# Kernel optimization log

Hardware: AMD Instinct MI355X
Metric: run time of the kernel (lower is better)

## Reference

```python
import jax, jax.numpy as jnp
import numpy as np

EPS = 1e-5
NEG_SLOPE = 0.2

def _bn(x, g, be, m, v):
    # inference-mode BatchNorm1d over the channel (last) dim
    return (x - m) * jax.lax.rsqrt(v + EPS) * g + be

def _lrelu(x):
    return jnp.where(x >= 0, x, NEG_SLOPE * x)

def setup_inputs() -> dict:
    key = jax.random.key(0)
    ks = jax.random.split(key, 32)
    B, N, M = 2, 65536, 16
    C_RAW, C_IN, C_RO, C_NB, C_OUT = 10, 32, 32, 64, 64
    i = iter(range(32))
    def nrm(shape, s=1.0):
        return jax.random.normal(ks[next(i)], shape, dtype=jnp.float32) * s
    def pos(shape):
        return jax.random.uniform(ks[next(i)], shape, dtype=jnp.float32)
    inp = {}
    inp['feature'] = nrm((B, N, C_IN))
    inp['raw_nb_fea'] = nrm((B, N, M, C_RAW))
    inp['neighbors_idx'] = jax.random.randint(ks[next(i)], (B, N, M), 0, N, dtype=jnp.int32)
    inp['w_raw'] = nrm((C_RAW, C_RO), 0.3); inp['b_raw'] = nrm((C_RO,), 0.1)
    inp['g_raw'] = pos((C_RO,)); inp['be_raw'] = nrm((C_RO,), 0.1)
    inp['m_raw'] = nrm((C_RO,), 0.1); inp['v_raw'] = pos((C_RO,))
    inp['w_nb'] = nrm((C_NB, C_NB), 0.15); inp['b_nb'] = nrm((C_NB,), 0.1)
    inp['g_nb'] = pos((C_NB,)); inp['be_nb'] = nrm((C_NB,), 0.1)
    inp['m_nb'] = nrm((C_NB,), 0.1); inp['v_nb'] = pos((C_NB,))
    inp['w_attn'] = nrm((C_NB, C_NB), 0.15)
    inp['w_out'] = nrm((C_NB, C_OUT), 0.15); inp['b_out'] = nrm((C_OUT,), 0.1)
    inp['g_out'] = pos((C_OUT,)); inp['be_out'] = nrm((C_OUT,), 0.1)
    inp['m_out'] = nrm((C_OUT,), 0.1); inp['v_out'] = pos((C_OUT,))
    inp['w_sc'] = nrm((C_IN, C_OUT), 0.3); inp['b_sc'] = nrm((C_OUT,), 0.1)
    inp['g_sc'] = pos((C_OUT,)); inp['be_sc'] = nrm((C_OUT,), 0.1)
    inp['m_sc'] = nrm((C_OUT,), 0.1); inp['v_sc'] = pos((C_OUT,))
    return inp

def reference(feature, raw_nb_fea, neighbors_idx,
              w_raw, b_raw, g_raw, be_raw, m_raw, v_raw,
              w_nb, b_nb, g_nb, be_nb, m_nb, v_nb,
              w_attn,
              w_out, b_out, g_out, be_out, m_out, v_out,
              w_sc, b_sc, g_sc, be_sc, m_sc, v_sc):
    B = feature.shape[0]
    # mlp_raw_neighbor_fea: (B,N,M,10) -> (B,N,M,32)
    raw_mlp = _lrelu(_bn(raw_nb_fea @ w_raw + b_raw, g_raw, be_raw, m_raw, v_raw))
    # index_points: gather neighbor features (B,N,M,C_in)
    b_idx = jnp.arange(B)[:, None, None]
    nb_fea = feature[b_idx, neighbors_idx]  # (B,N,M,32)
    cat = jnp.concatenate([nb_fea, raw_mlp], axis=3)  # (B,N,M,64)
    # mlp_neighbor_fea
    h = _lrelu(_bn(cat @ w_nb + b_nb, g_nb, be_nb, m_nb, v_nb))  # (B,N,M,64)
    # attention pooling over neighbor dim M
    attn = jax.nn.softmax(h @ w_attn, axis=2)
    pooled = jnp.sum(attn * h, axis=2)  # (B,N,64)
    # out + shortcut, leaky_relu
    out = _bn(pooled @ w_out + b_out, g_out, be_out, m_out, v_out)
    sc = _bn(feature @ w_sc + b_sc, g_sc, be_sc, m_sc, v_sc)
    return _lrelu(sc + out)
```

## Files before the change

### kernel.cpp

```cpp
#include <hip/hip_runtime.h>
#include <hip/hip_bf16.h>

typedef unsigned short u16;
typedef unsigned int u32;
typedef __attribute__((ext_vector_type(8))) short short8;
typedef __attribute__((ext_vector_type(4))) float f32x4;

typedef float __attribute__((may_alias)) f32a;
typedef __attribute__((ext_vector_type(2))) float f32x2_t;
typedef f32x2_t __attribute__((may_alias)) f32x2a;
typedef __attribute__((ext_vector_type(4))) float f32x4_t;
typedef f32x4_t __attribute__((may_alias)) f32x4a;
typedef __attribute__((ext_vector_type(2))) u32 u32x2_t;
typedef u32x2_t __attribute__((may_alias)) u32x2a;
typedef short8 __attribute__((may_alias)) short8a;

#define NSLOPE 0.2f
#define BNEPS  1e-5f
#define LOG2E  1.4426950408889634f

union U8 { short8 s; u16 u[8]; u32 w[4]; };

__device__ __forceinline__ u16 f2bf_scalar(float f) {
    union { float f; u32 i; } x; x.f = f;
    u32 u = x.i + 0x7FFFu + ((x.i >> 16) & 1u);
    return (u16)(u >> 16);
}

__device__ __forceinline__ u32 cvt2(float a, float b) {
#if __has_builtin(__builtin_amdgcn_cvt_pk_bf16_f32)
    auto p = __builtin_amdgcn_cvt_pk_bf16_f32(a, b);
    u32 w; __builtin_memcpy(&w, &p, sizeof(u32));
    return w;
#else
    return (u32)f2bf_scalar(a) | ((u32)f2bf_scalar(b) << 16);
#endif
}
__device__ __forceinline__ u16 cvt1(float a) { return (u16)cvt2(a, a); }

__device__ __forceinline__ float lrelu(float x) { return fmaxf(x, NSLOPE * x); }

__device__ __forceinline__ float fexp2(float x) {
#if __has_builtin(__builtin_amdgcn_exp2f)
    return __builtin_amdgcn_exp2f(x);
#else
    return exp2f(x);
#endif
}

__device__ __forceinline__ float ldf(const void* p, size_t i) { return ((const f32a*)p)[i]; }

__device__ __forceinline__ short8 load_bfrag(const void* W, int K, int Cn, int ks, int nt,
                                             int q, int t, float scale) {
    U8 x;
#pragma unroll
    for (int j = 0; j < 8; ++j) {
        int k = ks * 32 + q * 8 + j;
        x.u[j] = (k < K) ? f2bf_scalar(ldf(W, (size_t)k * Cn + nt * 16 + t) * scale) : (u16)0;
    }
    return x.s;
}

__device__ __forceinline__ short8 lds_afrag(const u16* buf, int row, int ks, int q) {
    const u16* cp = buf + row * 68 + ks * 32 + q * 8;
    u32x2a a = *(const u32x2a*)cp;
    u32x2a b = *(const u32x2a*)(cp + 4);
    U8 x; x.w[0] = a.x; x.w[1] = a.y; x.w[2] = b.x; x.w[3] = b.y;
    return x.s;
}

__device__ __forceinline__ short8 lds_wfrag(const u16* w, int n, int ks, int q) {
    int slot = ((ks << 2) | q) ^ (n & 7);
    return *(const short8a*)(w + (n << 6) + (slot << 3));
}

#define MFMA(a, b, c) __builtin_amdgcn_mfma_f32_16x16x32_bf16((a), (b), (c), 0, 0, 0)

__global__ __launch_bounds__(256, 4) void lfa_kernel(
    const void* __restrict__ feat,
    const void* __restrict__ rawf,
    const int*  __restrict__ nbidx,
    const void* __restrict__ w_raw,
    const void* __restrict__ b_raw, const void* __restrict__ g_raw,
    const void* __restrict__ be_raw, const void* __restrict__ m_raw,
    const void* __restrict__ v_raw,
    const void* __restrict__ w_nb,
    const void* __restrict__ b_nb, const void* __restrict__ g_nb,
    const void* __restrict__ be_nb, const void* __restrict__ m_nb,
    const void* __restrict__ v_nb,
    const void* __restrict__ w_attn,
    const void* __restrict__ w_out,
    const void* __restrict__ b_out, const void* __restrict__ g_out,
    const void* __restrict__ be_out, const void* __restrict__ m_out,
    const void* __restrict__ v_out,
    const void* __restrict__ w_sc,
    const void* __restrict__ b_sc, const void* __restrict__ g_sc,
    const void* __restrict__ be_sc, const void* __restrict__ m_sc,
    const void* __restrict__ v_sc,
    float* __restrict__ outp)
{
    __shared__ __align__(16) u16 s_cat[4][16 * 68];
    __shared__ __align__(16) u16 s_pool[4][16 * 68];
    __shared__ __align__(16) u16 s_wnbT[64 * 64];
    __shared__ __align__(16) u16 s_wattT[64 * 64];
    __shared__ float2 s_pr_raw[32];
    __shared__ float2 s_pr_nb[64];
    __shared__ float2 s_pr_out[64];
    __shared__ float2 s_pr_sc[64];

    const int tid  = threadIdx.x;
    const int lane = tid & 63;
    const int wv   = tid >> 6;
    const int t    = lane & 15;
    const int q    = lane >> 4;

    if (tid < 64) {
        int c = tid;
        float s = ldf(g_nb, c) * rsqrtf(ldf(v_nb, c) + BNEPS);
        s_pr_nb[c] = make_float2(s, (ldf(b_nb, c) - ldf(m_nb, c)) * s + ldf(be_nb, c));
    } else if (tid < 128) {
        int c = tid - 64;
        float s = ldf(g_out, c) * rsqrtf(ldf(v_out, c) + BNEPS);
        s_pr_out[c] = make_float2(s, (ldf(b_out, c) - ldf(m_out, c)) * s + ldf(be_out, c));
    } else if (tid < 192) {
        int c = tid - 128;
        float s = ldf(g_sc, c) * rsqrtf(ldf(v_sc, c) + BNEPS);
        s_pr_sc[c] = make_float2(s, (ldf(b_sc, c) - ldf(m_sc, c)) * s + ldf(be_sc, c));
    } else if (tid < 224) {
        int c = tid - 192;
        float s = ldf(g_raw, c) * rsqrtf(ldf(v_raw, c) + BNEPS);
        s_pr_raw[c] = make_float2(s, (ldf(b_raw, c) - ldf(m_raw, c)) * s + ldf(be_raw, c));
    }
    __syncthreads();

#pragma unroll 4
    for (int idx = tid; idx < 64 * 64; idx += 256) {
        int n = idx & 63, k = idx >> 6;
        int off = (n << 6) | (((k >> 3) ^ (n & 7)) << 3) | (k & 7);
        s_wnbT[off]  = f2bf_scalar(ldf(w_nb,   (size_t)k * 64 + n) * s_pr_nb[n].x);
        s_wattT[off] = f2bf_scalar(ldf(w_attn, (size_t)k * 64 + n) * LOG2E);
    }
    __syncthreads();

    short8 wraw[2];
    float bias_nb[4];
#pragma unroll
    for (int nt = 0; nt < 2; ++nt) {
        int c = nt * 16 + t;
        float2 pr = s_pr_raw[c];
        U8 x;
#pragma unroll
        for (int j = 0; j < 8; ++j) {
            int k = q * 8 + j;
            float v = (k < 10) ? ldf(w_raw, (size_t)k * 32 + c) * pr.x
                               : (k == 10 ? pr.y : 0.f);
            x.u[j] = f2bf_scalar(v);
        }
        wraw[nt] = x.s;
    }
#pragma unroll
    for (int nt = 0; nt < 4; ++nt) bias_nb[nt] = s_pr_nb[nt * 16 + t].y;

    u16* catw  = &s_cat[wv][0];
    u16* poolw = &s_pool[wv][0];

    const f32x4 zf = {0.f, 0.f, 0.f, 0.f};
    const int g  = blockIdx.x * 4 + wv;
    const int P0 = g * 16;
    const int bb = P0 >> 16;
    const size_t fb = (size_t)bb << 16;

    const int m_ = lane >> 2;
    const int pc = lane & 3;

    const int*  nbp  = nbidx + P0 * 16 + m_;
    const f32a* rawp = (const f32a*)rawf + (size_t)P0 * 160 + (size_t)t * 10;
    const float* fpb = (const float*)feat;

    auto load_gather = [&](int ix, f32x4& a, f32x4& b) {
        const float* fp = fpb + (fb + (size_t)ix) * 32 + pc * 8;
        a = *(const f32x4a*)fp;
        b = *(const f32x4a*)(fp + 4);
    };
    auto load_raw = [&](int p, f32x4& a, f32x4& b) {
        const f32a* rp = rawp + (size_t)p * 160;
        f32x2a r01 = *(const f32x2a*)rp;
        f32x2a r23 = *(const f32x2a*)(rp + 2);
        f32x2a r45 = *(const f32x2a*)(rp + 4);
        f32x2a r67 = *(const f32x2a*)(rp + 6);
        f32x2a r89 = *(const f32x2a*)(rp + 8);
        float q0 = (q == 0) ? 1.f : 0.f;
        float q1 = (q == 1) ? 1.f : 0.f;
        a.x = q0 * r01.x + q1 * r89.x;
        a.y = q0 * r01.y + q1 * r89.y;
        a.z = q0 * r23.x + q1;
        a.w = q0 * r23.y;
        b.x = q0 * r45.x; b.y = q0 * r45.y;
        b.z = q0 * r67.x; b.w = q0 * r67.y;
    };

    u32x2_t gpa, gpb;
    u32 rp0, rp1, rp2, rp3;
    {
        int ixA = nbp[0];
        f32x4 g0, g1, r0, r1;
        load_gather(ixA, g0, g1);
        load_raw(0, r0, r1);
        gpa.x = cvt2(g0.x, g0.y); gpa.y = cvt2(g0.z, g0.w);
        gpb.x = cvt2(g1.x, g1.y); gpb.y = cvt2(g1.z, g1.w);
        rp0 = cvt2(r0.x, r0.y); rp1 = cvt2(r0.z, r0.w);
        rp2 = cvt2(r1.x, r1.y); rp3 = cvt2(r1.z, r1.w);
    }
    int ixB = nbp[16];
    int licm = 0;

#pragma unroll 1
    for (int p = 0; p < 16; ++p) {
        asm volatile("" : "+v"(licm));
        const u16* wnbT  = s_wnbT  + licm;
        const u16* wattT = s_wattT + licm;

        const int pn  = (p + 1 < 16) ? p + 1 : 15;
        const int pnn = (p + 2 < 16) ? p + 2 : 15;
        f32x4 gb0, gb1, rb0, rb1;
        load_gather(ixB, gb0, gb1);
        load_raw(pn, rb0, rb1);
        int ixC = nbp[pnn * 16];

        *(u32x2a*)(catw + m_ * 68 + pc * 8)     = gpa;
        *(u32x2a*)(catw + m_ * 68 + pc * 8 + 4) = gpb;

        {
            U8 au;
            au.w[0] = rp0; au.w[1] = rp1; au.w[2] = rp2; au.w[3] = rp3;
            short8 ar = au.s;
            f32x4 racc[2];
            racc[0] = MFMA(ar, wraw[0], zf);
            racc[1] = MFMA(ar, wraw[1], zf);
#pragma unroll
            for (int nt = 0; nt < 2; ++nt) {
                int c = nt * 16 + t;
#pragma unroll
                for (int r = 0; r < 4; ++r) {
                    float x = lrelu(racc[nt][r]);
                    catw[(q * 4 + r) * 68 + 32 + c] = cvt1(x);
                }
            }
        }

        short8 a0 = lds_afrag(catw, t, 0, q);
        short8 a1 = lds_afrag(catw, t, 1, q);
        float hv[4][4];
#pragma unroll
        for (int nt = 0; nt < 4; ++nt) {
            int n = nt * 16 + t;
            short8 b0 = lds_wfrag(wnbT, n, 0, q);
            short8 b1 = lds_wfrag(wnbT, n, 1, q);
            f32x4 a = {bias_nb[nt], bias_nb[nt], bias_nb[nt], bias_nb[nt]};
            a = MFMA(a0, b0, a);
            a = MFMA(a1, b1, a);
#pragma unroll
            for (int r = 0; r < 4; ++r) {
                hv[nt][r] = lrelu(a[r]);
                catw[(q * 4 + r) * 68 + nt * 16 + t] = cvt1(hv[nt][r]);
            }
        }

        short8 h0 = lds_afrag(catw, t, 0, q);
        short8 h1 = lds_afrag(catw, t, 1, q);
        float pooled[4];
#pragma unroll
        for (int nt = 0; nt < 4; ++nt) {
            int n = nt * 16 + t;
            short8 b0 = lds_wfrag(wattT, n, 0, q);
            short8 b1 = lds_wfrag(wattT, n, 1, q);
            f32x4 s = zf;
            s = MFMA(h0, b0, s);
            s = MFMA(h1, b1, s);
            float num = 0.f, den = 0.f;
#pragma unroll
            for (int r = 0; r < 4; ++r) {
                float e = fexp2(s[r]);
                num += e * hv[nt][r];
                den += e;
            }
            num += __shfl_xor(num, 16); den += __shfl_xor(den, 16);
            num += __shfl_xor(num, 32); den += __shfl_xor(den, 32);
            pooled[nt] = num / den;
        }
        float pv = (q == 0) ? pooled[0] : (q == 1) ? pooled[1]
                 : (q == 2) ? pooled[2] : pooled[3];
        poolw[p * 68 + q * 16 + t] = cvt1(pv);

        gpa.x = cvt2(gb0.x, gb0.y); gpa.y = cvt2(gb0.z, gb0.w);
        gpb.x = cvt2(gb1.x, gb1.y); gpb.y = cvt2(gb1.z, gb1.w);
        rp0 = cvt2(rb0.x, rb0.y); rp1 = cvt2(rb0.z, rb0.w);
        rp2 = cvt2(rb1.x, rb1.y); rp3 = cvt2(rb1.z, rb1.w);
        ixB = ixC;
    }

    short8 wout[2][4], wsc[4];
    float bias_os[4];
#pragma unroll
    for (int nt = 0; nt < 4; ++nt) {
        float2 po = s_pr_out[nt * 16 + t];
        float2 ps = s_pr_sc[nt * 16 + t];
        bias_os[nt] = po.y + ps.y;
#pragma unroll
        for (int ks = 0; ks < 2; ++ks)
            wout[ks][nt] = load_bfrag(w_out, 64, 64, ks, nt, q, t, po.x);
        wsc[nt] = load_bfrag(w_sc, 32, 64, 0, nt, q, t, ps.x);
    }

    short8 pf0 = lds_afrag(poolw, t, 0, q);
    short8 pf1 = lds_afrag(poolw, t, 1, q);
    U8 sxu;
    {
        const float* fp = fpb + (size_t)(P0 + t) * 32 + q * 8;
        f32x4a v0 = *(const f32x4a*)fp;
        f32x4a v1 = *(const f32x4a*)(fp + 4);
        sxu.w[0] = cvt2(v0.x, v0.y); sxu.w[1] = cvt2(v0.z, v0.w);
        sxu.w[2] = cvt2(v1.x, v1.y); sxu.w[3] = cvt2(v1.z, v1.w);
    }
    short8 scf = sxu.s;
#pragma unroll
    for (int nt = 0; nt < 4; ++nt) {
        f32x4 oa = {bias_os[nt], bias_os[nt], bias_os[nt], bias_os[nt]};
        oa = MFMA(pf0, wout[0][nt], oa);
        oa = MFMA(pf1, wout[1][nt], oa);
        f32x4 sa = MFMA(scf, wsc[nt], zf);
#pragma unroll
        for (int r = 0; r < 4; ++r)
            outp[(size_t)(P0 + q * 4 + r) * 64 + nt * 16 + t] = lrelu(oa[r] + sa[r]);
    }
}

extern "C" void kernel_launch(void* const* d_in, const int* in_sizes, int n_in,
                              void* d_out, int out_size, void* d_ws, size_t ws_size,
                              hipStream_t stream) {
    hipLaunchKernelGGL(lfa_kernel, dim3(2048), dim3(256), 0, stream,
                       d_in[0], d_in[1], (const int*)d_in[2],
                       d_in[3], d_in[4], d_in[5], d_in[6], d_in[7], d_in[8],
                       d_in[9], d_in[10], d_in[11], d_in[12], d_in[13], d_in[14],
                       d_in[15],
                       d_in[16], d_in[17], d_in[18], d_in[19], d_in[20], d_in[21],
                       d_in[22], d_in[23], d_in[24], d_in[25], d_in[26], d_in[27],
                       (float*)d_out);
}
```

Measured before the change: 297.9 us.

## Permute weight K-order for packed LDS stores, hoist fragment addresses, use rcp

Permutes the K rows of the transposed w_nb and w_attn tiles in LDS so each lane's MFMA outputs for adjacent column tiles land contiguously. The raw-MLP and hidden activations can then be written to LDS as packed 32- and 64-bit stores instead of scalar 16-bit stores. Per-lane weight fragment base addresses are hoisted out of the loop, and the bias is added after the MFMA rather than preloaded into the accumulator. The softmax division becomes a select plus a hardware reciprocal, and the raw-feature load drops one load and its multiplies. The approximate reciprocal may slightly change numerics, and the occupancy hint is expressed as waves_per_eu instead of a launch_bounds minimum.

Result: faster. 283.5 us (-4.8%).

```diff
diff --git a/kernel.cpp b/kernel.cpp
--- a/kernel.cpp
+++ b/kernel.cpp
@@ -7,6 +7,7 @@
 typedef __attribute__((ext_vector_type(4))) float f32x4;
 
 typedef float __attribute__((may_alias)) f32a;
+typedef u32 __attribute__((may_alias)) u32a;
 typedef __attribute__((ext_vector_type(2))) float f32x2_t;
 typedef f32x2_t __attribute__((may_alias)) f32x2a;
 typedef __attribute__((ext_vector_type(4))) float f32x4_t;
@@ -48,6 +49,14 @@
 #endif
 }
 
+__device__ __forceinline__ float frcp(float x) {
+#if __has_builtin(__builtin_amdgcn_rcpf)
+    return __builtin_amdgcn_rcpf(x);
+#else
+    return 1.f / x;
+#endif
+}
+
 __device__ __forceinline__ float ldf(const void* p, size_t i) { return ((const f32a*)p)[i]; }
 
 __device__ __forceinline__ short8 load_bfrag(const void* W, int K, int Cn, int ks, int nt,
@@ -69,14 +78,15 @@
     return x.s;
 }
 
-__device__ __forceinline__ short8 lds_wfrag(const u16* w, int n, int ks, int q) {
-    int slot = ((ks << 2) | q) ^ (n & 7);
-    return *(const short8a*)(w + (n << 6) + (slot << 3));
+__device__ __forceinline__ short8 lds_wfrag2(const u16* base, int nt) {
+    return *(const short8a*)(base + (nt << 10));
 }
 
 #define MFMA(a, b, c) __builtin_amdgcn_mfma_f32_16x16x32_bf16((a), (b), (c), 0, 0, 0)
 
-__global__ __launch_bounds__(256, 4) void lfa_kernel(
+__global__ __launch_bounds__(256)
+__attribute__((amdgpu_waves_per_eu(4, 4)))
+void lfa_kernel(
     const void* __restrict__ feat,
     const void* __restrict__ rawf,
     const int*  __restrict__ nbidx,
@@ -135,10 +145,12 @@
 
 #pragma unroll 4
     for (int idx = tid; idx < 64 * 64; idx += 256) {
-        int n = idx & 63, k = idx >> 6;
-        int off = (n << 6) | (((k >> 3) ^ (n & 7)) << 3) | (k & 7);
-        s_wnbT[off]  = f2bf_scalar(ldf(w_nb,   (size_t)k * 64 + n) * s_pr_nb[n].x);
-        s_wattT[off] = f2bf_scalar(ldf(w_attn, (size_t)k * 64 + n) * LOG2E);
+        int n = idx & 63, s = idx >> 6;
+        int off = (n << 6) | (((s >> 3) ^ (n & 7)) << 3) | (s & 7);
+        int knb = (s < 32) ? s : 32 + (((s - 32) & 1) << 4) + ((s - 32) >> 1);
+        int kat = ((s & 3) << 4) + (s >> 2);
+        s_wnbT[off]  = f2bf_scalar(ldf(w_nb,   (size_t)knb * 64 + n) * s_pr_nb[n].x);
+        s_wattT[off] = f2bf_scalar(ldf(w_attn, (size_t)kat * 64 + n) * LOG2E);
     }
     __syncthreads();
 
@@ -161,6 +173,15 @@
 #pragma unroll
     for (int nt = 0; nt < 4; ++nt) bias_nb[nt] = s_pr_nb[nt * 16 + t].y;
 
+    const u16* wnb_base[2];
+    const u16* watt_base[2];
+#pragma unroll
+    for (int ks = 0; ks < 2; ++ks) {
+        int lane_off = (t << 6) + ((((ks << 2) | q) ^ (t & 7)) << 3);
+        wnb_base[ks]  = s_wnbT  + lane_off;
+        watt_base[ks] = s_wattT + lane_off;
+    }
+
     u16* catw  = &s_cat[wv][0];
     u16* poolw = &s_pool[wv][0];
 
@@ -176,6 +197,8 @@
     const int*  nbp  = nbidx + P0 * 16 + m_;
     const f32a* rawp = (const f32a*)rawf + (size_t)P0 * 160 + (size_t)t * 10;
     const float* fpb = (const float*)feat;
+
+    const bool q_lt2 = (q < 2), q_eq0 = (q == 0), q_eq1 = (q == 1);
 
     auto load_gather = [&](int ix, f32x4& a, f32x4& b) {
         const float* fp = fpb + (fb + (size_t)ix) * 32 + pc * 8;
@@ -184,19 +207,16 @@
     };
     auto load_raw = [&](int p, f32x4& a, f32x4& b) {
         const f32a* rp = rawp + (size_t)p * 160;
-        f32x2a r01 = *(const f32x2a*)rp;
-        f32x2a r23 = *(const f32x2a*)(rp + 2);
-        f32x2a r45 = *(const f32x2a*)(rp + 4);
-        f32x2a r67 = *(const f32x2a*)(rp + 6);
-        f32x2a r89 = *(const f32x2a*)(rp + 8);
-        float q0 = (q == 0) ? 1.f : 0.f;
-        float q1 = (q == 1) ? 1.f : 0.f;
-        a.x = q0 * r01.x + q1 * r89.x;
-        a.y = q0 * r01.y + q1 * r89.y;
-        a.z = q0 * r23.x + q1;
-        a.w = q0 * r23.y;
-        b.x = q0 * r45.x; b.y = q0 * r45.y;
-        b.z = q0 * r67.x; b.w = q0 * r67.y;
+        f32x2a L0 = *(const f32x2a*)(rp + ((q & 1) << 3));
+        f32x2a L1 = *(const f32x2a*)(rp + 2);
+        f32x2a L2 = *(const f32x2a*)(rp + 4);
+        f32x2a L3 = *(const f32x2a*)(rp + 6);
+        a.x = q_lt2 ? L0.x : 0.f;
+        a.y = q_lt2 ? L0.y : 0.f;
+        a.z = q_eq0 ? L1.x : (q_eq1 ? 1.f : 0.f);
+        a.w = q_eq0 ? L1.y : 0.f;
+        b.x = q_eq0 ? L2.x : 0.f;  b.y = q_eq0 ? L2.y : 0.f;
+        b.z = q_eq0 ? L3.x : 0.f;  b.w = q_eq0 ? L3.y : 0.f;
     };
 
     u32x2_t gpa, gpb;
@@ -217,8 +237,6 @@
 #pragma unroll 1
     for (int p = 0; p < 16; ++p) {
         asm volatile("" : "+v"(licm));
-        const u16* wnbT  = s_wnbT  + licm;
-        const u16* wattT = s_wattT + licm;
 
         const int pn  = (p + 1 < 16) ? p + 1 : 15;
         const int pnn = (p + 2 < 16) ? p + 2 : 15;
@@ -234,49 +252,44 @@
             U8 au;
             au.w[0] = rp0; au.w[1] = rp1; au.w[2] = rp2; au.w[3] = rp3;
             short8 ar = au.s;
-            f32x4 racc[2];
-            racc[0] = MFMA(ar, wraw[0], zf);
-            racc[1] = MFMA(ar, wraw[1], zf);
-#pragma unroll
-            for (int nt = 0; nt < 2; ++nt) {
-                int c = nt * 16 + t;
-#pragma unroll
-                for (int r = 0; r < 4; ++r) {
-                    float x = lrelu(racc[nt][r]);
-                    catw[(q * 4 + r) * 68 + 32 + c] = cvt1(x);
-                }
+            f32x4 racc0 = MFMA(ar, wraw[0], zf);
+            f32x4 racc1 = MFMA(ar, wraw[1], zf);
+#pragma unroll
+            for (int r = 0; r < 4; ++r) {
+                u32 wpk = cvt2(lrelu(racc0[r]), lrelu(racc1[r]));
+                *(u32a*)(catw + (q * 4 + r) * 68 + 32 + 2 * t) = wpk;
             }
         }
 
         short8 a0 = lds_afrag(catw, t, 0, q);
         short8 a1 = lds_afrag(catw, t, 1, q);
+        const u16* wb0 = wnb_base[0] + licm;
+        const u16* wb1 = wnb_base[1] + licm;
         float hv[4][4];
 #pragma unroll
         for (int nt = 0; nt < 4; ++nt) {
-            int n = nt * 16 + t;
-            short8 b0 = lds_wfrag(wnbT, n, 0, q);
-            short8 b1 = lds_wfrag(wnbT, n, 1, q);
-            f32x4 a = {bias_nb[nt], bias_nb[nt], bias_nb[nt], bias_nb[nt]};
-            a = MFMA(a0, b0, a);
-            a = MFMA(a1, b1, a);
-#pragma unroll
-            for (int r = 0; r < 4; ++r) {
-                hv[nt][r] = lrelu(a[r]);
-                catw[(q * 4 + r) * 68 + nt * 16 + t] = cvt1(hv[nt][r]);
-            }
+            f32x4 a = MFMA(a0, lds_wfrag2(wb0, nt), zf);
+            a = MFMA(a1, lds_wfrag2(wb1, nt), a);
+#pragma unroll
+            for (int r = 0; r < 4; ++r) hv[nt][r] = lrelu(a[r] + bias_nb[nt]);
+        }
+#pragma unroll
+        for (int r = 0; r < 4; ++r) {
+            u32x2_t w2;
+            w2.x = cvt2(hv[0][r], hv[1][r]);
+            w2.y = cvt2(hv[2][r], hv[3][r]);
+            *(u32x2a*)(catw + (q * 4 + r) * 68 + 4 * t) = w2;
         }
 
         short8 h0 = lds_afrag(catw, t, 0, q);
         short8 h1 = lds_afrag(catw, t, 1, q);
-        float pooled[4];
+        const u16* wa0 = watt_base[0] + licm;
+        const u16* wa1 = watt_base[1] + licm;
+        float pvn = 0.f, pvd = 1.f;
 #pragma unroll
         for (int nt = 0; nt < 4; ++nt) {
-            int n = nt * 16 + t;
-            short8 b0 = lds_wfrag(wattT, n, 0, q);
-            short8 b1 = lds_wfrag(wattT, n, 1, q);
-            f32x4 s = zf;
-            s = MFMA(h0, b0, s);
-            s = MFMA(h1, b1, s);
+            f32x4 s = MFMA(h0, lds_wfrag2(wa0, nt), zf);
+            s = MFMA(h1, lds_wfrag2(wa1, nt), s);
             float num = 0.f, den = 0.f;
 #pragma unroll
             for (int r = 0; r < 4; ++r) {
@@ -286,11 +299,11 @@
             }
             num += __shfl_xor(num, 16); den += __shfl_xor(den, 16);
             num += __shfl_xor(num, 32); den += __shfl_xor(den, 32);
-            pooled[nt] = num / den;
-        }
-        float pv = (q == 0) ? pooled[0] : (q == 1) ? pooled[1]
-                 : (q == 2) ? pooled[2] : pooled[3];
-        poolw[p * 68 + q * 16 + t] = cvt1(pv);
+            bool sel = (q == nt);
+            pvn = sel ? num : pvn;
+            pvd = sel ? den : pvd;
+        }
+        poolw[p * 68 + q * 16 + t] = cvt1(pvn * frcp(pvd));
 
         gpa.x = cvt2(gb0.x, gb0.y); gpa.y = cvt2(gb0.z, gb0.w);
         gpb.x = cvt2(gb1.x, gb1.y); gpb.y = cvt2(gb1.z, gb1.w);
```
